# Kernel tuning notes

Measured on AMD Instinct MI355X. Metric: run time of the kernel, lower is better.

## Reference

```python
import jax, jax.numpy as jnp
import numpy as np

B, N = 64, 512          # batch (Multiple*BatchSize), nodes per graph
LIT, SEM = 128, 64      # literal / semantic feature widths
ED, HD, OD = 64, 32, 64 # EmbedDim, HalfDim (hardcoded 32), OutputDim
ITERS, ELAYERS = 5, 2   # IteraTimes, EmbedLayer


def setup_inputs() -> dict:
    key = jax.random.key(0)
    ks = jax.random.split(key, 32)
    s = 0.05
    inp = {
        "cfg1": jax.random.randint(ks[0], (B, N, N), 0, 2, dtype=jnp.int32),
        "pfg1": jax.random.randint(ks[1], (B, N, N), 0, 2, dtype=jnp.int32),
        "lit1": jax.random.normal(ks[2], (B, N, LIT), dtype=jnp.float32),
        "sem1": jax.random.normal(ks[3], (B, N, SEM), dtype=jnp.float32),
        "cfg2": jax.random.randint(ks[4], (B, N, N), 0, 2, dtype=jnp.int32),
        "pfg2": jax.random.randint(ks[5], (B, N, N), 0, 2, dtype=jnp.int32),
        "lit2": jax.random.normal(ks[6], (B, N, LIT), dtype=jnp.float32),
        "sem2": jax.random.normal(ks[7], (B, N, SEM), dtype=jnp.float32),
    }
    # branch 1 (MyDataLayer #1) params
    inp["d1w1"] = jax.random.normal(ks[8], (LIT, ED)) * s
    inp["d1b1"] = jnp.zeros((ED,), jnp.float32)
    inp["d2w1"] = jax.random.normal(ks[9], (ED, HD)) * s
    inp["d2b1"] = jnp.zeros((HD,), jnp.float32)
    inp["lk1"] = jax.random.normal(ks[10], (SEM, 4 * HD)) * s
    inp["lrk1"] = jax.random.normal(ks[11], (HD, 4 * HD)) * s
    inp["lb1"] = jnp.zeros((4 * HD,), jnp.float32)
    # branch 2 (MyDataLayer #2) params
    inp["d1w2"] = jax.random.normal(ks[12], (LIT, ED)) * s
    inp["d1b2"] = jnp.zeros((ED,), jnp.float32)
    inp["d2w2"] = jax.random.normal(ks[13], (ED, HD)) * s
    inp["d2b2"] = jnp.zeros((HD,), jnp.float32)
    inp["lk2"] = jax.random.normal(ks[14], (SEM, 4 * HD)) * s
    inp["lrk2"] = jax.random.normal(ks[15], (HD, 4 * HD)) * s
    inp["lb2"] = jnp.zeros((4 * HD,), jnp.float32)
    # shared MyEmbedLayer params
    inp["we_w"] = jax.random.normal(ks[16], (ELAYERS, ED, ED)) * s
    inp["we_b"] = jnp.zeros((ELAYERS, ED), jnp.float32)
    inp["wout"] = jax.random.normal(ks[17], (ED, OD)) * s
    inp["bout"] = jnp.zeros((OD,), jnp.float32)
    return inp


def _lstm(x, k, rk, b):
    # x: [B, T, D]; Keras gate order i, f, c(g), o; sigmoid recurrent activation
    h0 = jnp.zeros((x.shape[0], rk.shape[0]), x.dtype)

    def step(carry, xt):
        h, c = carry
        z = xt @ k + h @ rk + b
        i, f, g, o = jnp.split(z, 4, axis=-1)
        c = jax.nn.sigmoid(f) * c + jax.nn.sigmoid(i) * jnp.tanh(g)
        h = jax.nn.sigmoid(o) * jnp.tanh(c)
        return (h, c), h

    _, hs = jax.lax.scan(step, (h0, h0), jnp.swapaxes(x, 0, 1))
    return jnp.swapaxes(hs, 0, 1)  # [B, T, HD]


def _branch(lit, sem, d1w, d1b, d2w, d2b, lk, lrk, lb):
    mlp = jax.nn.relu(jax.nn.relu(lit @ d1w + d1b) @ d2w + d2b)  # [B,N,HD]
    return jnp.concatenate([mlp, _lstm(sem, lk, lrk, lb)], axis=-1)  # [B,N,ED]


def _embed(inp, adj, we_w, we_b, wout, bout):
    x = jax.nn.relu(inp)
    for _ in range(ITERS):
        t = adj @ x  # [B,N,N] @ [B,N,ED] -> message passing
        for l in range(ELAYERS):
            t = jax.nn.relu(t @ we_w[l] + we_b[l])
        x = jnp.tanh(inp + t)
    return x.sum(axis=1) @ wout + bout  # [B, OD]


def reference(cfg1, pfg1, lit1, sem1, cfg2, pfg2, lit2, sem2,
              d1w1, d1b1, d2w1, d2b1, lk1, lrk1, lb1,
              d1w2, d1b2, d2w2, d2b2, lk2, lrk2, lb2,
              we_w, we_b, wout, bout):
    bb1 = _branch(lit1, sem1, d1w1, d1b1, d2w1, d2b1, lk1, lrk1, lb1)
    e1 = _embed(bb1, cfg1.astype(jnp.float32), we_w, we_b, wout, bout)
    bb2 = _branch(lit2, sem2, d1w2, d1b2, d2w2, d2b2, lk2, lrk2, lb2)
    e2 = _embed(bb2, cfg2.astype(jnp.float32), we_w, we_b, wout, bout)
    num = jnp.sum(e1 * e2, axis=1)
    den = jnp.sqrt(jnp.sum(e1 ** 2, axis=1) * jnp.sum(e2 ** 2, axis=1) + 1e-10)
    return num / den  # [B]
```

## Files before the change

### kernel.cpp

```cpp
#include <hip/hip_runtime.h>

#define DEV static __device__ __forceinline__

typedef float  f32x2 __attribute__((ext_vector_type(2)));
typedef float  f32x4 __attribute__((ext_vector_type(4)));
typedef float  f32x8 __attribute__((ext_vector_type(8)));
typedef __bf16 bf16x8 __attribute__((ext_vector_type(8)));
typedef unsigned short u16x8 __attribute__((ext_vector_type(8)));

DEV unsigned short f2bf(float f) {
  unsigned u = __builtin_bit_cast(unsigned, f);
  u += 0x7FFFu + ((u >> 16) & 1u);
  return (unsigned short)(u >> 16);
}
DEV float bf2f(unsigned short h) {
  unsigned u = (unsigned)h << 16;
  return __builtin_bit_cast(float, u);
}

DEV f32x4 mfma16(u16x8 a, u16x8 b, f32x4 c) {
  return __builtin_amdgcn_mfma_f32_16x16x32_bf16(
      __builtin_bit_cast(bf16x8, a), __builtin_bit_cast(bf16x8, b), c, 0, 0, 0);
}

DEV float tanh_f(float x) {
  x = fminf(fmaxf(x, -20.f), 20.f);
  float e = __expf(2.f * x);
  return (e - 1.f) * __builtin_amdgcn_rcpf(e + 1.f);
}

DEV float exp2_hw(float x) { float r; asm("v_exp_f32 %0, %1" : "=v"(r) : "v"(x)); return r; }
DEV float sig_fast(float x) { return __builtin_amdgcn_rcpf(1.f + exp2_hw(-1.44269504f * x)); }
DEV float tanh_fast(float x) { return 1.f - 2.f * __builtin_amdgcn_rcpf(exp2_hw(2.88539008f * x) + 1.f); }

DEV void pkfma(f32x2& acc, f32x2 a, f32x2 b) {
  asm("v_pk_fma_f32 %0, %1, %2, %0" : "+v"(acc) : "v"(a), "v"(b));
}

DEV u16x8 byte2bf(unsigned byte) {
  union { unsigned u[4]; u16x8 v; } r;
  #pragma unroll
  for (int i = 0; i < 4; ++i) {
    unsigned b0 = (byte >> (2 * i)) & 1u;
    unsigned b1 = (byte >> (2 * i + 1)) & 1u;
    r.u[i] = (b0 ? 0x3F80u : 0u) | (b1 ? 0x3F800000u : 0u);
  }
  return r.v;
}

DEV void split8(const float* p, u16x8& h, u16x8& l) {
  union { f32x4 q[2]; f32x8 o; } u;
  u.q[0] = *reinterpret_cast<const f32x4*>(p);
  u.q[1] = *reinterpret_cast<const f32x4*>(p + 4);
  #pragma unroll
  for (int i = 0; i < 8; ++i) {
    float v = u.o[i];
    unsigned short hb = f2bf(v);
    h[i] = hb;
    l[i] = f2bf(v - bf2f(hb));
  }
}

template <int K, int NC, int ACT>
__global__ __launch_bounds__(256) void k_ff(
    const float* __restrict__ A1, const float* __restrict__ A2,
    const float* __restrict__ W1, const float* __restrict__ W2,
    const float* __restrict__ b1, const float* __restrict__ b2,
    float* __restrict__ C, int ldC, long brCstride) {
  int bid = blockIdx.x;
  int br = bid >> 8, rbk = bid & 255;
  const float* A = br ? A2 : A1;
  const float* W = br ? W2 : W1;
  const float* bias = br ? b2 : b1;

  __shared__ __attribute__((aligned(16))) unsigned short WTh[NC][K + 8];
  __shared__ __attribute__((aligned(16))) unsigned short WTl[NC][K + 8];
  for (int idx = threadIdx.x; idx < K * NC; idx += 256) {
    int k = idx / NC, c = idx % NC;
    float w = W[idx];
    unsigned short hb = f2bf(w);
    WTh[c][k] = hb;
    WTl[c][k] = f2bf(w - bf2f(hb));
  }
  __syncthreads();

  int wave = threadIdx.x >> 6, lane = threadIdx.x & 63;
  int l15 = lane & 15, g = lane >> 4;
  int row0 = rbk * 128 + wave * 32;

  f32x4 acc[2][NC / 16] = {};
  for (int kk = 0; kk < K; kk += 32) {
    u16x8 ah[2], al[2];
    #pragma unroll
    for (int rt = 0; rt < 2; ++rt)
      split8(A + (size_t)(row0 + rt * 16 + l15) * K + kk + g * 8, ah[rt], al[rt]);
    #pragma unroll
    for (int ct = 0; ct < NC / 16; ++ct) {
      u16x8 wh = *reinterpret_cast<const u16x8*>(&WTh[ct * 16 + l15][kk + g * 8]);
      u16x8 wl = *reinterpret_cast<const u16x8*>(&WTl[ct * 16 + l15][kk + g * 8]);
      #pragma unroll
      for (int rt = 0; rt < 2; ++rt) {
        acc[rt][ct] = mfma16(ah[rt], wh, acc[rt][ct]);
        acc[rt][ct] = mfma16(al[rt], wh, acc[rt][ct]);
        acc[rt][ct] = mfma16(ah[rt], wl, acc[rt][ct]);
      }
    }
  }

  float bv[NC / 16];
  #pragma unroll
  for (int ct = 0; ct < NC / 16; ++ct) bv[ct] = bias[ct * 16 + l15];
  #pragma unroll
  for (int rt = 0; rt < 2; ++rt)
    #pragma unroll
    for (int ct = 0; ct < NC / 16; ++ct)
      #pragma unroll
      for (int r = 0; r < 4; ++r) {
        float v = acc[rt][ct][r] + bv[ct];
        if (ACT) v = fmaxf(v, 0.f);
        C[(size_t)br * brCstride +
          (size_t)(row0 + rt * 16 + g * 4 + r) * ldC + ct * 16 + l15] = v;
      }
}

__global__ __launch_bounds__(256) void k_front(
    const float* __restrict__ xk,
    const float* __restrict__ lrk1, const float* __restrict__ lrk2,
    float* __restrict__ bb,
    const int* __restrict__ cfg1, const int* __restrict__ cfg2,
    unsigned* __restrict__ bits,
    const float* __restrict__ lit1, const float* __restrict__ lit2,
    const float* __restrict__ d1w1, const float* __restrict__ d1w2,
    const float* __restrict__ d1b1, const float* __restrict__ d1b2,
    const float* __restrict__ d2w1, const float* __restrict__ d2w2,
    const float* __restrict__ d2b1, const float* __restrict__ d2b2) {
  __shared__ __attribute__((aligned(16))) unsigned short WT1h[64][136];
  __shared__ __attribute__((aligned(16))) unsigned short WT1l[64][136];
  __shared__ __attribute__((aligned(16))) unsigned short WT2h[32][72];
  __shared__ __attribute__((aligned(16))) unsigned short WT2l[32][72];
  __shared__ __attribute__((aligned(16))) float H1[128][68];
  __shared__ __attribute__((aligned(16))) float sh[4][64];

  int bid = blockIdx.x;
  int wave = threadIdx.x >> 6, lane = threadIdx.x & 63;

  if (bid < 32) {
    int gb = bid * 4 + wave;
    int br = gb >> 6, b = gb & 63;
    int u = lane & 31, hi = lane >> 5;
    int c0 = u + (hi << 5), c1 = c0 + 64;
    const float* rkp = br ? lrk2 : lrk1;
    f32x2 rk0p[16], rk1p[16];
    #pragma unroll
    for (int k2 = 0; k2 < 16; ++k2) {
      rk0p[k2] = f32x2{rkp[(2 * k2) * 128 + c0], rkp[(2 * k2 + 1) * 128 + c0]};
      rk1p[k2] = f32x2{rkp[(2 * k2) * 128 + c1], rkp[(2 * k2 + 1) * 128 + c1]};
    }
    float* shw = &sh[wave][0];
    shw[lane] = 0.f;

    const float* xkb = xk + ((size_t)br * 32768 + (size_t)b * 512) * 128;
    float* bbo = bb + ((size_t)br * 32768 + (size_t)b * 512) * 64 + 32;
    float cst = 0.f;

    float z00 = xkb[0 * 128 + c0], z10 = xkb[0 * 128 + c1];
    float z01 = xkb[1 * 128 + c0], z11 = xkb[1 * 128 + c1];
    float z02 = xkb[2 * 128 + c0], z12 = xkb[2 * 128 + c1];
    float z03 = xkb[3 * 128 + c0], z13 = xkb[3 * 128 + c1];
    float z04 = xkb[4 * 128 + c0], z14 = xkb[4 * 128 + c1];
    float z05 = xkb[5 * 128 + c0], z15 = xkb[5 * 128 + c1];
    float z06 = xkb[6 * 128 + c0], z16 = xkb[6 * 128 + c1];
    float z07 = xkb[7 * 128 + c0], z17 = xkb[7 * 128 + c1];

    union Q { f32x4 q; f32x2 p[2]; };

#define LSTM_STEP(T, ZA, ZB) {                                          \
    float a0 = ZA, a1 = ZB;                                             \
    ZA = xkb[((T) + 8) * 128 + c0]; ZB = xkb[((T) + 8) * 128 + c1];     \
    Q q0, q1, q2, q3, q4, q5, q6, q7;                                   \
    q0.q = *reinterpret_cast<const f32x4*>(&shw[32]);                   \
    q1.q = *reinterpret_cast<const f32x4*>(&shw[36]);                   \
    q2.q = *reinterpret_cast<const f32x4*>(&shw[40]);                   \
    q3.q = *reinterpret_cast<const f32x4*>(&shw[44]);                   \
    q4.q = *reinterpret_cast<const f32x4*>(&shw[48]);                   \
    q5.q = *reinterpret_cast<const f32x4*>(&shw[52]);                   \
    q6.q = *reinterpret_cast<const f32x4*>(&shw[56]);                   \
    q7.q = *reinterpret_cast<const f32x4*>(&shw[60]);                   \
    f32x2 A0 = {0.f, 0.f}, A1 = {0.f, 0.f};                             \
    f32x2 B0 = {0.f, 0.f}, B1 = {0.f, 0.f};                             \
    pkfma(A0, q0.p[0], rk0p[0]);  pkfma(B0, q0.p[0], rk1p[0]);          \
    pkfma(A1, q0.p[1], rk0p[1]);  pkfma(B1, q0.p[1], rk1p[1]);          \
    pkfma(A0, q1.p[0], rk0p[2]);  pkfma(B0, q1.p[0], rk1p[2]);          \
    pkfma(A1, q1.p[1], rk0p[3]);  pkfma(B1, q1.p[1], rk1p[3]);          \
    pkfma(A0, q2.p[0], rk0p[4]);  pkfma(B0, q2.p[0], rk1p[4]);          \
    pkfma(A1, q2.p[1], rk0p[5]);  pkfma(B1, q2.p[1], rk1p[5]);          \
    pkfma(A0, q3.p[0], rk0p[6]);  pkfma(B0, q3.p[0], rk1p[6]);          \
    pkfma(A1, q3.p[1], rk0p[7]);  pkfma(B1, q3.p[1], rk1p[7]);          \
    pkfma(A0, q4.p[0], rk0p[8]);  pkfma(B0, q4.p[0], rk1p[8]);          \
    pkfma(A1, q4.p[1], rk0p[9]);  pkfma(B1, q4.p[1], rk1p[9]);          \
    pkfma(A0, q5.p[0], rk0p[10]); pkfma(B0, q5.p[0], rk1p[10]);         \
    pkfma(A1, q5.p[1], rk0p[11]); pkfma(B1, q5.p[1], rk1p[11]);         \
    pkfma(A0, q6.p[0], rk0p[12]); pkfma(B0, q6.p[0], rk1p[12]);         \
    pkfma(A1, q6.p[1], rk0p[13]); pkfma(B1, q6.p[1], rk1p[13]);         \
    pkfma(A0, q7.p[0], rk0p[14]); pkfma(B0, q7.p[0], rk1p[14]);         \
    pkfma(A1, q7.p[1], rk0p[15]); pkfma(B1, q7.p[1], rk1p[15]);         \
    float a0f = a0 + (A0.x + A1.x) + (A0.y + A1.y);                     \
    float a1f = a1 + (B0.x + B1.x) + (B0.y + B1.y);                     \
    float s0 = sig_fast(a0f);                     \
    float s1 = hi ? sig_fast(a1f) : tanh_fast(a1f);  \
    float at = s0 * s1;                           \
    float rc = __shfl_xor(at, 32);                                      \
    cst = s0 * cst + rc;                          \
    float hv = s1 * tanh_fast(cst);                                     \
    shw[lane] = hv;                                                     \
    if (hi) bbo[(T) * 64 + u] = hv;                                     \
  }

    for (int tb = 0; tb < 512; tb += 8) {
      LSTM_STEP(tb + 0, z00, z10)
      LSTM_STEP(tb + 1, z01, z11)
      LSTM_STEP(tb + 2, z02, z12)
      LSTM_STEP(tb + 3, z03, z13)
      LSTM_STEP(tb + 4, z04, z14)
      LSTM_STEP(tb + 5, z05, z15)
      LSTM_STEP(tb + 6, z06, z16)
      LSTM_STEP(tb + 7, z07, z17)
    }
#undef LSTM_STEP
    return;
  }

  if (bid < 288) {
    unsigned worker = (unsigned)(bid - 32) * 256u + threadIdx.x;
    #pragma unroll
    for (int j = 0; j < 16; ++j) {
      unsigned idx = worker + (unsigned)j * 65536u;
      unsigned br2 = idx >> 19;
      unsigned rem = idx & 524287u;
      const int4* p = reinterpret_cast<const int4*>(br2 ? cfg2 : cfg1) + rem * 8;
      unsigned m = 0;
      #pragma unroll
      for (int q = 0; q < 8; ++q) {
        int4 v = p[q];
        unsigned base = q * 4;
        m |= ((unsigned)v.x & 1u) << (base + 0);
        m |= ((unsigned)v.y & 1u) << (base + 1);
        m |= ((unsigned)v.z & 1u) << (base + 2);
        m |= ((unsigned)v.w & 1u) << (base + 3);
      }
      bits[idx] = m;
    }
    return;
  }

  int bid2 = bid - 288;
  int br = bid2 >> 8, rbk = bid2 & 255;
  const float* lit = br ? lit2 : lit1;
  const float* W1  = br ? d1w2 : d1w1;
  const float* B1  = br ? d1b2 : d1b1;
  const float* W2  = br ? d2w2 : d2w1;
  const float* B2  = br ? d2b2 : d2b1;

  for (int idx = threadIdx.x; idx < 8192; idx += 256) {
    int k = idx >> 6, c = idx & 63;
    float w = W1[idx];
    unsigned short hb = f2bf(w);
    WT1h[c][k] = hb;
    WT1l[c][k] = f2bf(w - bf2f(hb));
  }
  for (int idx = threadIdx.x; idx < 2048; idx += 256) {
    int k = idx >> 5, c = idx & 31;
    float w = W2[idx];
    unsigned short hb = f2bf(w);
    WT2h[c][k] = hb;
    WT2l[c][k] = f2bf(w - bf2f(hb));
  }
  __syncthreads();

  int l15 = lane & 15, g = lane >> 4;
  int row0 = rbk * 128 + wave * 32;

  f32x4 acc[2][4] = {};
  #pragma unroll
  for (int kk = 0; kk < 128; kk += 32) {
    u16x8 ah[2], al[2];
    #pragma unroll
    for (int rt = 0; rt < 2; ++rt)
      split8(lit + (size_t)(row0 + rt * 16 + l15) * 128 + kk + g * 8, ah[rt], al[rt]);
    #pragma unroll
    for (int ct = 0; ct < 4; ++ct) {
      u16x8 wh = *reinterpret_cast<const u16x8*>(&WT1h[ct * 16 + l15][kk + g * 8]);
      u16x8 wl = *reinterpret_cast<const u16x8*>(&WT1l[ct * 16 + l15][kk + g * 8]);
      #pragma unroll
      for (int rt = 0; rt < 2; ++rt) {
        acc[rt][ct] = mfma16(ah[rt], wh, acc[rt][ct]);
        acc[rt][ct] = mfma16(al[rt], wh, acc[rt][ct]);
        acc[rt][ct] = mfma16(ah[rt], wl, acc[rt][ct]);
      }
    }
  }
  #pragma unroll
  for (int ct = 0; ct < 4; ++ct) {
    float bv = B1[ct * 16 + l15];
    #pragma unroll
    for (int rt = 0; rt < 2; ++rt)
      #pragma unroll
      for (int r = 0; r < 4; ++r)
        H1[wave * 32 + rt * 16 + g * 4 + r][ct * 16 + l15] =
            fmaxf(acc[rt][ct][r] + bv, 0.f);
  }
  f32x4 acc2[2][2] = {};
  #pragma unroll
  for (int kk = 0; kk < 64; kk += 32) {
    u16x8 ah[2], al[2];
    #pragma unroll
    for (int rt = 0; rt < 2; ++rt)
      split8(&H1[wave * 32 + rt * 16 + l15][kk + g * 8], ah[rt], al[rt]);
    #pragma unroll
    for (int ct = 0; ct < 2; ++ct) {
      u16x8 wh = *reinterpret_cast<const u16x8*>(&WT2h[ct * 16 + l15][kk + g * 8]);
      u16x8 wl = *reinterpret_cast<const u16x8*>(&WT2l[ct * 16 + l15][kk + g * 8]);
      #pragma unroll
      for (int rt = 0; rt < 2; ++rt) {
        acc2[rt][ct] = mfma16(ah[rt], wh, acc2[rt][ct]);
        acc2[rt][ct] = mfma16(al[rt], wh, acc2[rt][ct]);
        acc2[rt][ct] = mfma16(ah[rt], wl, acc2[rt][ct]);
      }
    }
  }
  #pragma unroll
  for (int ct = 0; ct < 2; ++ct) {
    float bv = B2[ct * 16 + l15];
    #pragma unroll
    for (int rt = 0; rt < 2; ++rt)
      #pragma unroll
      for (int r = 0; r < 4; ++r)
        bb[((size_t)br * 32768 + row0 + rt * 16 + g * 4 + r) * 64 + ct * 16 + l15] =
            fmaxf(acc2[rt][ct][r] + bv, 0.f);
  }
}

__global__ __launch_bounds__(256) void k_relu_t(const float* __restrict__ bb,
                                                unsigned short* __restrict__ XTh,
                                                unsigned short* __restrict__ XTl) {
  int bid = blockIdx.x;
  int br = bid >> 9, rem = bid & 511, b = rem >> 3, tile = rem & 7;
  int n0 = tile * 64;
  __shared__ unsigned short xh[64][65], xl[64][65];
  const f32x4* src =
      reinterpret_cast<const f32x4*>(bb + ((size_t)(br * 64 + b) * 512 + n0) * 64);
  #pragma unroll
  for (int i = 0; i < 4; ++i) {
    int f = i * 256 + threadIdx.x;
    f32x4 v = src[f];
    int n = f >> 4, c4 = (f & 15) * 4;
    #pragma unroll
    for (int j = 0; j < 4; ++j) {
      float val = fmaxf(v[j], 0.f);
      unsigned short hb = f2bf(val);
      xh[n][c4 + j] = hb;
      xl[n][c4 + j] = f2bf(val - bf2f(hb));
    }
  }
  __syncthreads();
  int c = threadIdx.x >> 2, j0 = (threadIdx.x & 3) * 16;
  size_t base = ((size_t)(br * 64 + b) * 64 + c) * 512 + n0 + j0;
  u16x8 o0, o1, p0, p1;
  #pragma unroll
  for (int i = 0; i < 8; ++i) {
    o0[i] = xh[j0 + i][c]; o1[i] = xh[j0 + 8 + i][c];
    p0[i] = xl[j0 + i][c]; p1[i] = xl[j0 + 8 + i][c];
  }
  *reinterpret_cast<u16x8*>(XTh + base) = o0;
  *reinterpret_cast<u16x8*>(XTh + base + 8) = o1;
  *reinterpret_cast<u16x8*>(XTl + base) = p0;
  *reinterpret_cast<u16x8*>(XTl + base + 8) = p1;
}

template <int LAST>
__global__ __launch_bounds__(256, 2) void k_iter(
    const unsigned* __restrict__ bits,
    const unsigned short* __restrict__ XTh_in,
    const unsigned short* __restrict__ XTl_in,
    const float* __restrict__ bb,
    const float* __restrict__ we_w, const float* __restrict__ we_b,
    unsigned short* __restrict__ XTh_out, unsigned short* __restrict__ XTl_out,
    float* __restrict__ Spart) {
  int bid = blockIdx.x;
  int rb = bid >> 7, br = (bid >> 6) & 1, b = bid & 63;
  int n0 = rb * 256;
  __shared__ __attribute__((aligned(16))) unsigned short WT0h[64][72];
  __shared__ __attribute__((aligned(16))) unsigned short WT0l[64][72];
  __shared__ __attribute__((aligned(16))) unsigned short WT1h[64][72];
  __shared__ __attribute__((aligned(16))) unsigned short WT1l[64][72];
  __shared__ __attribute__((aligned(16))) char uni[34816];
  __shared__ float colsum[16][64];
  auto ts = reinterpret_cast<float(*)[32][68]>(uni);
  auto xh = reinterpret_cast<unsigned short(*)[65]>(uni);
  auto xl = reinterpret_cast<unsigned short(*)[65]>(uni + 16640);

  for (int idx = threadIdx.x; idx < 4096; idx += 256) {
    int k = idx >> 6, c = idx & 63;
    float w0 = we_w[k * 64 + c], w1 = we_w[4096 + k * 64 + c];
    unsigned short h0 = f2bf(w0), h1b = f2bf(w1);
    WT0h[c][k] = h0; WT0l[c][k] = f2bf(w0 - bf2f(h0));
    WT1h[c][k] = h1b; WT1l[c][k] = f2bf(w1 - bf2f(h1b));
  }
  __syncthreads();

  int wave = threadIdx.x >> 6, lane = threadIdx.x & 63;
  int l15 = lane & 15, g = lane >> 4;
  int rowbase = n0 + wave * 64;

  union BWU { uint4 v[4]; unsigned w[16]; };
  BWU bw0, bw1, bw2, bw3;
  {
    const unsigned* p0 =
        bits + (size_t)br * 524288 + ((size_t)b * 512 + rowbase + l15) * 16;
    #pragma unroll
    for (int q = 0; q < 4; ++q) {
      bw0.v[q] = reinterpret_cast<const uint4*>(p0)[q];
      bw1.v[q] = reinterpret_cast<const uint4*>(p0 + 256)[q];
      bw2.v[q] = reinterpret_cast<const uint4*>(p0 + 512)[q];
      bw3.v[q] = reinterpret_cast<const uint4*>(p0 + 768)[q];
    }
  }
  size_t xtbase = (size_t)(br * 64 + b) * 64 * 512;

  f32x4 acc[4][4] = {};
  #pragma unroll
  for (int kk = 0; kk < 512; kk += 32) {
    u16x8 a0 = byte2bf((bw0.w[kk >> 5] >> (g * 8)) & 0xFFu);
    u16x8 a1 = byte2bf((bw1.w[kk >> 5] >> (g * 8)) & 0xFFu);
    u16x8 a2 = byte2bf((bw2.w[kk >> 5] >> (g * 8)) & 0xFFu);
    u16x8 a3 = byte2bf((bw3.w[kk >> 5] >> (g * 8)) & 0xFFu);
    #pragma unroll
    for (int ct = 0; ct < 4; ++ct) {
      size_t off = xtbase + (size_t)(ct * 16 + l15) * 512 + kk + g * 8;
      u16x8 bh = *reinterpret_cast<const u16x8*>(XTh_in + off);
      u16x8 bl = *reinterpret_cast<const u16x8*>(XTl_in + off);
      acc[0][ct] = mfma16(a0, bh, acc[0][ct]);
      acc[0][ct] = mfma16(a0, bl, acc[0][ct]);
      acc[1][ct] = mfma16(a1, bh, acc[1][ct]);
      acc[1][ct] = mfma16(a1, bl, acc[1][ct]);
      acc[2][ct] = mfma16(a2, bh, acc[2][ct]);
      acc[2][ct] = mfma16(a2, bl, acc[2][ct]);
      acc[3][ct] = mfma16(a3, bh, acc[3][ct]);
      acc[3][ct] = mfma16(a3, bl, acc[3][ct]);
    }
  }

  float sacc[4] = {0.f, 0.f, 0.f, 0.f};

  #pragma unroll
  for (int p = 0; p < 2; ++p) {
    if (!LAST && p) __syncthreads();

    #pragma unroll
    for (int rt = 0; rt < 2; ++rt)
      #pragma unroll
      for (int ct = 0; ct < 4; ++ct)
        #pragma unroll
        for (int r = 0; r < 4; ++r)
          ts[wave][rt * 16 + g * 4 + r][ct * 16 + l15] = acc[2 * p + rt][ct][r];

    f32x4 acc1[2][4] = {};
    #pragma unroll
    for (int kk = 0; kk < 64; kk += 32) {
      u16x8 ah[2], al[2];
      #pragma unroll
      for (int rt = 0; rt < 2; ++rt)
        split8(&ts[wave][rt * 16 + l15][kk + g * 8], ah[rt], al[rt]);
      #pragma unroll
      for (int ct = 0; ct < 4; ++ct) {
        u16x8 wh = *reinterpret_cast<const u16x8*>(&WT0h[ct * 16 + l15][kk + g * 8]);
        u16x8 wl = *reinterpret_cast<const u16x8*>(&WT0l[ct * 16 + l15][kk + g * 8]);
        #pragma unroll
        for (int rt = 0; rt < 2; ++rt) {
          acc1[rt][ct] = mfma16(ah[rt], wh, acc1[rt][ct]);
          acc1[rt][ct] = mfma16(al[rt], wh, acc1[rt][ct]);
          acc1[rt][ct] = mfma16(ah[rt], wl, acc1[rt][ct]);
        }
      }
    }
    #pragma unroll
    for (int rt = 0; rt < 2; ++rt)
      #pragma unroll
      for (int ct = 0; ct < 4; ++ct) {
        float bv = we_b[ct * 16 + l15];
        #pragma unroll
        for (int r = 0; r < 4; ++r)
          ts[wave][rt * 16 + g * 4 + r][ct * 16 + l15] =
              fmaxf(acc1[rt][ct][r] + bv, 0.f);
      }

    f32x4 acc2[2][4] = {};
    #pragma unroll
    for (int kk = 0; kk < 64; kk += 32) {
      u16x8 ah[2], al[2];
      #pragma unroll
      for (int rt = 0; rt < 2; ++rt)
        split8(&ts[wave][rt * 16 + l15][kk + g * 8], ah[rt], al[rt]);
      #pragma unroll
      for (int ct = 0; ct < 4; ++ct) {
        u16x8 wh = *reinterpret_cast<const u16x8*>(&WT1h[ct * 16 + l15][kk + g * 8]);
        u16x8 wl = *reinterpret_cast<const u16x8*>(&WT1l[ct * 16 + l15][kk + g * 8]);
        #pragma unroll
        for (int rt = 0; rt < 2; ++rt) {
          acc2[rt][ct] = mfma16(ah[rt], wh, acc2[rt][ct]);
          acc2[rt][ct] = mfma16(al[rt], wh, acc2[rt][ct]);
          acc2[rt][ct] = mfma16(ah[rt], wl, acc2[rt][ct]);
        }
      }
    }

    const float* bbrow =
        bb + ((size_t)(br * 64 + b) * 512 + rowbase + p * 32) * 64;

    if (!LAST) {
      __syncthreads();
      #pragma unroll
      for (int rt = 0; rt < 2; ++rt)
        #pragma unroll
        for (int ct = 0; ct < 4; ++ct) {
          float bv = we_b[64 + ct * 16 + l15];
          #pragma unroll
          for (int r = 0; r < 4; ++r) {
            int rr = rt * 16 + g * 4 + r, cc = ct * 16 + l15;
            float t3 = fmaxf(acc2[rt][ct][r] + bv, 0.f);
            float v = tanh_f(bbrow[rr * 64 + cc] + t3);
            unsigned short hb = f2bf(v);
            xh[wave * 32 + rr][cc] = hb;
            xl[wave * 32 + rr][cc] = f2bf(v - bf2f(hb));
          }
        }
      __syncthreads();
      int c = threadIdx.x >> 2, w4 = threadIdx.x & 3;
      int j0 = w4 * 32;
      size_t base = ((size_t)(br * 64 + b) * 64 + c) * 512 + n0 + w4 * 64 + p * 32;
      u16x8 o0, o1, o2, o3, q0, q1, q2, q3;
      #pragma unroll
      for (int i = 0; i < 8; ++i) {
        o0[i] = xh[j0 + i][c];      o1[i] = xh[j0 + 8 + i][c];
        o2[i] = xh[j0 + 16 + i][c]; o3[i] = xh[j0 + 24 + i][c];
        q0[i] = xl[j0 + i][c];      q1[i] = xl[j0 + 8 + i][c];
        q2[i] = xl[j0 + 16 + i][c]; q3[i] = xl[j0 + 24 + i][c];
      }
      *reinterpret_cast<u16x8*>(XTh_out + base) = o0;
      *reinterpret_cast<u16x8*>(XTh_out + base + 8) = o1;
      *reinterpret_cast<u16x8*>(XTh_out + base + 16) = o2;
      *reinterpret_cast<u16x8*>(XTh_out + base + 24) = o3;
      *reinterpret_cast<u16x8*>(XTl_out + base) = q0;
      *reinterpret_cast<u16x8*>(XTl_out + base + 8) = q1;
      *reinterpret_cast<u16x8*>(XTl_out + base + 16) = q2;
      *reinterpret_cast<u16x8*>(XTl_out + base + 24) = q3;
    } else {
      #pragma unroll
      for (int ct = 0; ct < 4; ++ct) {
        float bv = we_b[64 + ct * 16 + l15];
        float s = 0.f;
        #pragma unroll
        for (int rt = 0; rt < 2; ++rt)
          #pragma unroll
          for (int r = 0; r < 4; ++r) {
            int rr = rt * 16 + g * 4 + r, cc = ct * 16 + l15;
            float t3 = fmaxf(acc2[rt][ct][r] + bv, 0.f);
            s += tanh_f(bbrow[rr * 64 + cc] + t3);
          }
        sacc[ct] += s;
      }
    }
  }

  if (LAST) {
    #pragma unroll
    for (int ct = 0; ct < 4; ++ct)
      colsum[wave * 4 + g][ct * 16 + l15] = sacc[ct];
    __syncthreads();
    if (threadIdx.x < 64) {
      float s = 0.f;
      #pragma unroll
      for (int q = 0; q < 16; ++q) s += colsum[q][threadIdx.x];
      Spart[((size_t)(br * 64 + b) * 2 + rb) * 64 + threadIdx.x] = s;
    }
  }
}

__global__ __launch_bounds__(64) void k_final(const float* __restrict__ Spart,
                                              const float* __restrict__ wout,
                                              const float* __restrict__ bout,
                                              float* __restrict__ out) {
  int b = blockIdx.x, c = threadIdx.x;
  __shared__ float s1s[64], s2s[64];
  float s1 = 0.f, s2 = 0.f;
  #pragma unroll
  for (int tl = 0; tl < 2; ++tl) {
    s1 += Spart[((size_t)(0 * 64 + b) * 2 + tl) * 64 + c];
    s2 += Spart[((size_t)(1 * 64 + b) * 2 + tl) * 64 + c];
  }
  s1s[c] = s1; s2s[c] = s2;
  __syncthreads();
  float e1 = bout[c], e2 = bout[c];
  for (int k = 0; k < 64; ++k) {
    float w = wout[k * 64 + c];
    e1 += s1s[k] * w;
    e2 += s2s[k] * w;
  }
  float nm = e1 * e2, dA = e1 * e1, dB = e2 * e2;
  #pragma unroll
  for (int off = 32; off; off >>= 1) {
    nm += __shfl_xor(nm, off);
    dA += __shfl_xor(dA, off);
    dB += __shfl_xor(dB, off);
  }
  if (c == 0) out[b] = nm / sqrtf(dA * dB + 1e-10f);
}

extern "C" void kernel_launch(void* const* d_in, const int* in_sizes, int n_in,
                              void* d_out, int out_size, void* d_ws, size_t ws_size,
                              hipStream_t stream) {
  const int*   cfg1 = (const int*)d_in[0];
  const float* lit1 = (const float*)d_in[2];
  const float* sem1 = (const float*)d_in[3];
  const int*   cfg2 = (const int*)d_in[4];
  const float* lit2 = (const float*)d_in[6];
  const float* sem2 = (const float*)d_in[7];
  const float* d1w1 = (const float*)d_in[8];
  const float* d1b1 = (const float*)d_in[9];
  const float* d2w1 = (const float*)d_in[10];
  const float* d2b1 = (const float*)d_in[11];
  const float* lk1  = (const float*)d_in[12];
  const float* lrk1 = (const float*)d_in[13];
  const float* lb1  = (const float*)d_in[14];
  const float* d1w2 = (const float*)d_in[15];
  const float* d1b2 = (const float*)d_in[16];
  const float* d2w2 = (const float*)d_in[17];
  const float* d2b2 = (const float*)d_in[18];
  const float* lk2  = (const float*)d_in[19];
  const float* lrk2 = (const float*)d_in[20];
  const float* lb2  = (const float*)d_in[21];
  const float* we_w = (const float*)d_in[22];
  const float* we_b = (const float*)d_in[23];
  const float* wout = (const float*)d_in[24];
  const float* bout = (const float*)d_in[25];

  char* ws = (char*)d_ws;
  float* bb   = (float*)ws;
  float* xk   = (float*)(ws + 16777216);
  unsigned short* XTBh = (unsigned short*)(ws + 16777216);
  unsigned short* XTBl = (unsigned short*)(ws + 25165824);
  unsigned short* XTAl = (unsigned short*)(ws + 33554432);
  unsigned short* XTAh = (unsigned short*)(ws + 50331648);
  float* Spart = (float*)(ws + 58720256);
  unsigned* bits = (unsigned*)(ws + 58982400);

  k_ff<64, 128, 0><<<512, 256, 0, stream>>>(sem1, sem2, lk1, lk2, lb1, lb2,
                                            xk, 128, 4194304L);

  k_front<<<800, 256, 0, stream>>>(xk, lrk1, lrk2, bb, cfg1, cfg2, bits,
                                   lit1, lit2, d1w1, d1w2, d1b1, d1b2,
                                   d2w1, d2w2, d2b1, d2b2);

  k_relu_t<<<1024, 256, 0, stream>>>(bb, XTAh, XTAl);

  for (int it = 0; it < 5; ++it) {
    int p = it & 1;
    const unsigned short* ih = p ? XTBh : XTAh;
    const unsigned short* il = p ? XTBl : XTAl;
    unsigned short* oh = p ? XTAh : XTBh;
    unsigned short* ol = p ? XTAl : XTBl;
    if (it < 4)
      k_iter<0><<<256, 256, 0, stream>>>(bits, ih, il, bb, we_w, we_b, oh, ol, Spart);
    else
      k_iter<1><<<256, 256, 0, stream>>>(bits, ih, il, bb, we_w, we_b, oh, ol, Spart);
  }
  k_final<<<64, 64, 0, stream>>>(Spart, wout, bout, (float*)d_out);
}
```

Before: 356.5 us.

## Use int8 two-level quantized node states with i8 MFMA for adjacency aggregation

Iterations after the first now store the tanh-bounded node states as two int8 planes (a coarse value scaled by 127 plus a residual scaled by 127 again) instead of bf16 hi/lo planes. The adjacency matmul then runs on i8 16x16x64 MFMA, and the 0/1 adjacency bits are expanded straight to int8 bytes. This halves the bytes read and written for the state and doubles K per MFMA. The trade-off is a fixed quantization error of about 1/16129 in place of the bf16 split precision.

```diff
diff --git a/kernel.cpp b/kernel.cpp
--- a/kernel.cpp
+++ b/kernel.cpp
@@ -7,6 +7,7 @@
 typedef float  f32x8 __attribute__((ext_vector_type(8)));
 typedef __bf16 bf16x8 __attribute__((ext_vector_type(8)));
 typedef unsigned short u16x8 __attribute__((ext_vector_type(8)));
+typedef int    i32x4 __attribute__((ext_vector_type(4)));
 
 DEV unsigned short f2bf(float f) {
   unsigned u = __builtin_bit_cast(unsigned, f);
@@ -22,6 +23,10 @@
   return __builtin_amdgcn_mfma_f32_16x16x32_bf16(
       __builtin_bit_cast(bf16x8, a), __builtin_bit_cast(bf16x8, b), c, 0, 0, 0);
 }
+DEV i32x4 mfma8(uint4 a, uint4 b, i32x4 c) {
+  return __builtin_amdgcn_mfma_i32_16x16x64_i8(
+      __builtin_bit_cast(i32x4, a), __builtin_bit_cast(i32x4, b), c, 0, 0, 0);
+}
 
 DEV float tanh_f(float x) {
   x = fminf(fmaxf(x, -20.f), 20.f);
@@ -37,15 +42,13 @@
   asm("v_pk_fma_f32 %0, %1, %2, %0" : "+v"(acc) : "v"(a), "v"(b));
 }
 
-DEV u16x8 byte2bf(unsigned byte) {
-  union { unsigned u[4]; u16x8 v; } r;
-  #pragma unroll
-  for (int i = 0; i < 4; ++i) {
-    unsigned b0 = (byte >> (2 * i)) & 1u;
-    unsigned b1 = (byte >> (2 * i + 1)) & 1u;
-    r.u[i] = (b0 ? 0x3F80u : 0u) | (b1 ? 0x3F800000u : 0u);
-  }
-  return r.v;
+DEV uint4 expand16(unsigned hw) {
+  uint4 r;
+  r.x = ((hw         & 0xFu) * 0x00204081u) & 0x01010101u;
+  r.y = (((hw >> 4)  & 0xFu) * 0x00204081u) & 0x01010101u;
+  r.z = (((hw >> 8)  & 0xFu) * 0x00204081u) & 0x01010101u;
+  r.w = (((hw >> 12) & 0xFu) * 0x00204081u) & 0x01010101u;
+  return r;
 }
 
 DEV void split8(const float* p, u16x8& h, u16x8& l) {
@@ -377,14 +380,14 @@
   *reinterpret_cast<u16x8*>(XTl + base + 8) = p1;
 }
 
-template <int LAST>
+template <int AIN8, int LAST>
 __global__ __launch_bounds__(256, 2) void k_iter(
     const unsigned* __restrict__ bits,
-    const unsigned short* __restrict__ XTh_in,
-    const unsigned short* __restrict__ XTl_in,
+    const unsigned short* __restrict__ XTbfh, const unsigned short* __restrict__ XTbfl,
+    const char* __restrict__ X8h_in, const char* __restrict__ X8l_in,
     const float* __restrict__ bb,
     const float* __restrict__ we_w, const float* __restrict__ we_b,
-    unsigned short* __restrict__ XTh_out, unsigned short* __restrict__ XTl_out,
+    char* __restrict__ X8h_out, char* __restrict__ X8l_out,
     float* __restrict__ Spart) {
   int bid = blockIdx.x;
   int rb = bid >> 7, br = (bid >> 6) & 1, b = bid & 63;
@@ -395,9 +398,9 @@
   __shared__ __attribute__((aligned(16))) unsigned short WT1l[64][72];
   __shared__ __attribute__((aligned(16))) char uni[34816];
   __shared__ float colsum[16][64];
-  auto ts = reinterpret_cast<float(*)[32][68]>(uni);
-  auto xh = reinterpret_cast<unsigned short(*)[65]>(uni);
-  auto xl = reinterpret_cast<unsigned short(*)[65]>(uni + 16640);
+  auto ts  = reinterpret_cast<float(*)[32][68]>(uni);
+  auto xh8 = reinterpret_cast<char(*)[65]>(uni);
+  auto xl8 = reinterpret_cast<char(*)[65]>(uni + 8320);
 
   for (int idx = threadIdx.x; idx < 4096; idx += 256) {
     int k = idx >> 6, c = idx & 63;
@@ -425,29 +428,89 @@
       bw3.v[q] = reinterpret_cast<const uint4*>(p0 + 768)[q];
     }
   }
-  size_t xtbase = (size_t)(br * 64 + b) * 64 * 512;
-
-  f32x4 acc[4][4] = {};
-  #pragma unroll
-  for (int kk = 0; kk < 512; kk += 32) {
-    u16x8 a0 = byte2bf((bw0.w[kk >> 5] >> (g * 8)) & 0xFFu);
-    u16x8 a1 = byte2bf((bw1.w[kk >> 5] >> (g * 8)) & 0xFFu);
-    u16x8 a2 = byte2bf((bw2.w[kk >> 5] >> (g * 8)) & 0xFFu);
-    u16x8 a3 = byte2bf((bw3.w[kk >> 5] >> (g * 8)) & 0xFFu);
-    #pragma unroll
-    for (int ct = 0; ct < 4; ++ct) {
-      size_t off = xtbase + (size_t)(ct * 16 + l15) * 512 + kk + g * 8;
-      u16x8 bh = *reinterpret_cast<const u16x8*>(XTh_in + off);
-      u16x8 bl = *reinterpret_cast<const u16x8*>(XTl_in + off);
-      acc[0][ct] = mfma16(a0, bh, acc[0][ct]);
-      acc[0][ct] = mfma16(a0, bl, acc[0][ct]);
-      acc[1][ct] = mfma16(a1, bh, acc[1][ct]);
-      acc[1][ct] = mfma16(a1, bl, acc[1][ct]);
-      acc[2][ct] = mfma16(a2, bh, acc[2][ct]);
-      acc[2][ct] = mfma16(a2, bl, acc[2][ct]);
-      acc[3][ct] = mfma16(a3, bh, acc[3][ct]);
-      acc[3][ct] = mfma16(a3, bl, acc[3][ct]);
-    }
+
+  float tv[4][4][4];
+
+  if constexpr (!AIN8) {
+    size_t xtbase = (size_t)(br * 64 + b) * 64 * 512;
+    f32x4 acc[4][4] = {};
+    #pragma unroll
+    for (int kk = 0; kk < 512; kk += 32) {
+      u16x8 a0, a1, a2, a3;
+      {
+        unsigned w0 = bw0.w[kk >> 5] >> (g * 8), w1 = bw1.w[kk >> 5] >> (g * 8);
+        unsigned w2 = bw2.w[kk >> 5] >> (g * 8), w3 = bw3.w[kk >> 5] >> (g * 8);
+        union { unsigned u[4]; u16x8 v; } r0, r1, r2, r3;
+        #pragma unroll
+        for (int i = 0; i < 4; ++i) {
+          r0.u[i] = (((w0 >> (2 * i)) & 1u) ? 0x3F80u : 0u) |
+                    (((w0 >> (2 * i + 1)) & 1u) ? 0x3F800000u : 0u);
+          r1.u[i] = (((w1 >> (2 * i)) & 1u) ? 0x3F80u : 0u) |
+                    (((w1 >> (2 * i + 1)) & 1u) ? 0x3F800000u : 0u);
+          r2.u[i] = (((w2 >> (2 * i)) & 1u) ? 0x3F80u : 0u) |
+                    (((w2 >> (2 * i + 1)) & 1u) ? 0x3F800000u : 0u);
+          r3.u[i] = (((w3 >> (2 * i)) & 1u) ? 0x3F80u : 0u) |
+                    (((w3 >> (2 * i + 1)) & 1u) ? 0x3F800000u : 0u);
+        }
+        a0 = r0.v; a1 = r1.v; a2 = r2.v; a3 = r3.v;
+      }
+      #pragma unroll
+      for (int ct = 0; ct < 4; ++ct) {
+        size_t off = xtbase + (size_t)(ct * 16 + l15) * 512 + kk + g * 8;
+        u16x8 bh = *reinterpret_cast<const u16x8*>(XTbfh + off);
+        u16x8 bl = *reinterpret_cast<const u16x8*>(XTbfl + off);
+        acc[0][ct] = mfma16(a0, bh, acc[0][ct]);
+        acc[0][ct] = mfma16(a0, bl, acc[0][ct]);
+        acc[1][ct] = mfma16(a1, bh, acc[1][ct]);
+        acc[1][ct] = mfma16(a1, bl, acc[1][ct]);
+        acc[2][ct] = mfma16(a2, bh, acc[2][ct]);
+        acc[2][ct] = mfma16(a2, bl, acc[2][ct]);
+        acc[3][ct] = mfma16(a3, bh, acc[3][ct]);
+        acc[3][ct] = mfma16(a3, bl, acc[3][ct]);
+      }
+    }
+    #pragma unroll
+    for (int rt = 0; rt < 4; ++rt)
+      #pragma unroll
+      for (int ct = 0; ct < 4; ++ct)
+        #pragma unroll
+        for (int r = 0; r < 4; ++r)
+          tv[rt][ct][r] = acc[rt][ct][r];
+  } else {
+    size_t x8base = (size_t)(br * 64 + b) * 64 * 512;
+    i32x4 acch[4][4] = {};
+    i32x4 accl[4][4] = {};
+    #pragma unroll
+    for (int c64 = 0; c64 < 8; ++c64) {
+      int kk = c64 * 64;
+      int wi = (kk >> 5) + (g >> 1), shv = (g & 1) * 16;
+      uint4 a0 = expand16((bw0.w[wi] >> shv) & 0xFFFFu);
+      uint4 a1 = expand16((bw1.w[wi] >> shv) & 0xFFFFu);
+      uint4 a2 = expand16((bw2.w[wi] >> shv) & 0xFFFFu);
+      uint4 a3 = expand16((bw3.w[wi] >> shv) & 0xFFFFu);
+      #pragma unroll
+      for (int ct = 0; ct < 4; ++ct) {
+        size_t off = x8base + (size_t)(ct * 16 + l15) * 512 + kk + g * 16;
+        uint4 bh = *reinterpret_cast<const uint4*>(X8h_in + off);
+        uint4 bl = *reinterpret_cast<const uint4*>(X8l_in + off);
+        acch[0][ct] = mfma8(a0, bh, acch[0][ct]);
+        accl[0][ct] = mfma8(a0, bl, accl[0][ct]);
+        acch[1][ct] = mfma8(a1, bh, acch[1][ct]);
+        accl[1][ct] = mfma8(a1, bl, accl[1][ct]);
+        acch[2][ct] = mfma8(a2, bh, acch[2][ct]);
+        accl[2][ct] = mfma8(a2, bl, accl[2][ct]);
+        acch[3][ct] = mfma8(a3, bh, acch[3][ct]);
+        accl[3][ct] = mfma8(a3, bl, accl[3][ct]);
+      }
+    }
+    #pragma unroll
+    for (int rt = 0; rt < 4; ++rt)
+      #pragma unroll
+      for (int ct = 0; ct < 4; ++ct)
+        #pragma unroll
+        for (int r = 0; r < 4; ++r)
+          tv[rt][ct][r] = (float)acch[rt][ct][r] * (1.f / 127.f) +
+                          (float)accl[rt][ct][r] * (1.f / 16129.f);
   }
 
   float sacc[4] = {0.f, 0.f, 0.f, 0.f};
@@ -462,7 +525,7 @@
       for (int ct = 0; ct < 4; ++ct)
         #pragma unroll
         for (int r = 0; r < 4; ++r)
-          ts[wave][rt * 16 + g * 4 + r][ct * 16 + l15] = acc[2 * p + rt][ct][r];
+          ts[wave][rt * 16 + g * 4 + r][ct * 16 + l15] = tv[2 * p + rt][ct][r];
 
     f32x4 acc1[2][4] = {};
     #pragma unroll
@@ -529,31 +592,27 @@
             int rr = rt * 16 + g * 4 + r, cc = ct * 16 + l15;
             float t3 = fmaxf(acc2[rt][ct][r] + bv, 0.f);
             float v = tanh_f(bbrow[rr * 64 + cc] + t3);
-            unsigned short hb = f2bf(v);
-            xh[wave * 32 + rr][cc] = hb;
-            xl[wave * 32 + rr][cc] = f2bf(v - bf2f(hb));
+            float s = v * 127.f;
+            float qhf = rintf(s);
+            float qlf = rintf((s - qhf) * 127.f);
+            xh8[wave * 32 + rr][cc] = (char)(int)qhf;
+            xl8[wave * 32 + rr][cc] = (char)(int)qlf;
           }
         }
       __syncthreads();
       int c = threadIdx.x >> 2, w4 = threadIdx.x & 3;
       int j0 = w4 * 32;
       size_t base = ((size_t)(br * 64 + b) * 64 + c) * 512 + n0 + w4 * 64 + p * 32;
-      u16x8 o0, o1, o2, o3, q0, q1, q2, q3;
-      #pragma unroll
-      for (int i = 0; i < 8; ++i) {
-        o0[i] = xh[j0 + i][c];      o1[i] = xh[j0 + 8 + i][c];
-        o2[i] = xh[j0 + 16 + i][c]; o3[i] = xh[j0 + 24 + i][c];
-        q0[i] = xl[j0 + i][c];      q1[i] = xl[j0 + 8 + i][c];
-        q2[i] = xl[j0 + 16 + i][c]; q3[i] = xl[j0 + 24 + i][c];
-      }
-      *reinterpret_cast<u16x8*>(XTh_out + base) = o0;
-      *reinterpret_cast<u16x8*>(XTh_out + base + 8) = o1;
-      *reinterpret_cast<u16x8*>(XTh_out + base + 16) = o2;
-      *reinterpret_cast<u16x8*>(XTh_out + base + 24) = o3;
-      *reinterpret_cast<u16x8*>(XTl_out + base) = q0;
-      *reinterpret_cast<u16x8*>(XTl_out + base + 8) = q1;
-      *reinterpret_cast<u16x8*>(XTl_out + base + 16) = q2;
-      *reinterpret_cast<u16x8*>(XTl_out + base + 24) = q3;
+      union { uint4 v[2]; char bch[32]; } oh, ol;
+      #pragma unroll
+      for (int i = 0; i < 32; ++i) {
+        oh.bch[i] = xh8[j0 + i][c];
+        ol.bch[i] = xl8[j0 + i][c];
+      }
+      *reinterpret_cast<uint4*>(X8h_out + base) = oh.v[0];
+      *reinterpret_cast<uint4*>(X8h_out + base + 16) = oh.v[1];
+      *reinterpret_cast<uint4*>(X8l_out + base) = ol.v[0];
+      *reinterpret_cast<uint4*>(X8l_out + base + 16) = ol.v[1];
     } else {
       #pragma unroll
       for (int ct = 0; ct < 4; ++ct) {
@@ -647,10 +706,12 @@
   char* ws = (char*)d_ws;
   float* bb   = (float*)ws;
   float* xk   = (float*)(ws + 16777216);
-  unsigned short* XTBh = (unsigned short*)(ws + 16777216);
-  unsigned short* XTBl = (unsigned short*)(ws + 25165824);
-  unsigned short* XTAl = (unsigned short*)(ws + 33554432);
-  unsigned short* XTAh = (unsigned short*)(ws + 50331648);
+  unsigned short* XTbfh = (unsigned short*)(ws + 16777216);
+  unsigned short* XTbfl = (unsigned short*)(ws + 25165824);
+  char* A8h = ws + 33554432;
+  char* A8l = ws + 37748736;
+  char* B8h = ws + 41943040;
+  char* B8l = ws + 46137344;
   float* Spart = (float*)(ws + 58720256);
   unsigned* bits = (unsigned*)(ws + 58982400);
 
@@ -661,18 +722,18 @@
                                    lit1, lit2, d1w1, d1w2, d1b1, d1b2,
                                    d2w1, d2w2, d2b1, d2b2);
 
-  k_relu_t<<<1024, 256, 0, stream>>>(bb, XTAh, XTAl);
-
-  for (int it = 0; it < 5; ++it) {
-    int p = it & 1;
-    const unsigned short* ih = p ? XTBh : XTAh;
-    const unsigned short* il = p ? XTBl : XTAl;
-    unsigned short* oh = p ? XTAh : XTBh;
-    unsigned short* ol = p ? XTAl : XTBl;
-    if (it < 4)
-      k_iter<0><<<256, 256, 0, stream>>>(bits, ih, il, bb, we_w, we_b, oh, ol, Spart);
-    else
-      k_iter<1><<<256, 256, 0, stream>>>(bits, ih, il, bb, we_w, we_b, oh, ol, Spart);
-  }
+  k_relu_t<<<1024, 256, 0, stream>>>(bb, XTbfh, XTbfl);
+
+  k_iter<0, 0><<<256, 256, 0, stream>>>(bits, XTbfh, XTbfl, nullptr, nullptr,
+                                        bb, we_w, we_b, A8h, A8l, Spart);
+  k_iter<1, 0><<<256, 256, 0, stream>>>(bits, nullptr, nullptr, A8h, A8l,
+                                        bb, we_w, we_b, B8h, B8l, Spart);
+  k_iter<1, 0><<<256, 256, 0, stream>>>(bits, nullptr, nullptr, B8h, B8l,
+                                        bb, we_w, we_b, A8h, A8l, Spart);
+  k_iter<1, 0><<<256, 256, 0, stream>>>(bits, nullptr, nullptr, A8h, A8l,
+                                        bb, we_w, we_b, B8h, B8l, Spart);
+  k_iter<1, 1><<<256, 256, 0, stream>>>(bits, nullptr, nullptr, B8h, B8l,
+                                        bb, we_w, we_b, A8h, A8l, Spart);
+
   k_final<<<64, 64, 0, stream>>>(Spart, wout, bout, (float*)d_out);
 }
```

Result: faster. 332.0 us (-6.9%).
